# Optimization experiments

Measured on AMD Instinct MI355X. Metric: run time of the kernel, lower is better.

The kernel has to match this reference:

```python
import jax, jax.numpy as jnp
import numpy as np

B, N, K = 64, 128, 12
D_ATOM, D_NBR, D_NEW = 256, 320, 256
H, DK = 8, 32  # D_NEW = H * DK
LN_EPS = 1e-5
NEG_INF = -1e9


def setup_inputs() -> dict:
    key = jax.random.key(0)
    ks = jax.random.split(key, 10)
    atom_feature = jax.random.normal(ks[0], (B, N, D_ATOM), jnp.float32)
    atom_neighbor_feature = jax.random.normal(ks[1], (B, N, K, D_NBR), jnp.float32)
    # valid-neighbor masks from random neighbor counts in [1, K]
    counts = jax.random.randint(ks[2], (B, N), 1, K + 1)
    valid = (jnp.arange(K)[None, None, :] < counts[:, :, None]).astype(jnp.float32)
    atom_attend_mask = valid[..., None]                      # (B,N,K,1), 1=real neighbor
    atom_softmax_mask = (1.0 - valid[..., None]) * NEG_INF   # (B,N,K,1), additive
    # parameters
    s = 1.0 / np.sqrt(D_ATOM)
    W_atom = jax.random.uniform(ks[3], (D_ATOM, D_NEW), jnp.float32, -s, s)
    b_atom = jnp.zeros((D_NEW,), jnp.float32)
    s2 = 1.0 / np.sqrt(D_NBR)
    W_nbr = jax.random.uniform(ks[4], (D_NBR, D_NEW), jnp.float32, -s2, s2)
    b_nbr = jnp.zeros((D_NEW,), jnp.float32)
    s3 = 1.0 / np.sqrt(DK)
    w_align = jax.random.uniform(ks[5], (DK, 1), jnp.float32, -s3, s3)
    b_align = jnp.zeros((1,), jnp.float32)
    ln_gamma = jnp.ones((D_NEW,), jnp.float32)
    ln_beta = jnp.zeros((D_NEW,), jnp.float32)
    return dict(atom_feature=atom_feature, atom_neighbor_feature=atom_neighbor_feature,
                atom_softmax_mask=atom_softmax_mask, atom_attend_mask=atom_attend_mask,
                W_atom=W_atom, b_atom=b_atom, W_nbr=W_nbr, b_nbr=b_nbr,
                w_align=w_align, b_align=b_align, ln_gamma=ln_gamma, ln_beta=ln_beta)


def reference(atom_feature, atom_neighbor_feature, atom_softmax_mask, atom_attend_mask,
              W_atom, b_atom, W_nbr, b_nbr, w_align, b_align, ln_gamma, ln_beta):
    # dropout is identity at eval time
    h = atom_feature @ W_atom + b_atom                    # (B,N,D_NEW)
    e = atom_neighbor_feature @ W_nbr + b_nbr             # (B,N,K,D_NEW)
    h = h.reshape(B, N, 1, H, DK)                         # broadcast over K
    e = e.reshape(B, N, K, H, DK)
    # GATv2: act(h_i + e_j) then per-head linear score
    feat = jax.nn.leaky_relu(h + e)                       # slope 0.01 == torch default
    score = feat @ w_align + b_align                      # (B,N,K,H,1)
    score = score + atom_softmax_mask[:, :, :, None, :]   # additive -inf on pad
    attn = jax.nn.softmax(score, axis=2)                  # softmax over neighbors K
    attn = attn * atom_attend_mask[:, :, :, None, :]
    ctx = jnp.sum(attn * e, axis=2).reshape(B, N, H * DK)  # (B,N,D_NEW)
    # LayerNorm
    mu = jnp.mean(ctx, axis=-1, keepdims=True)
    xc = ctx - mu
    var = jnp.mean(xc * xc, axis=-1, keepdims=True)
    return xc * jax.lax.rsqrt(var + LN_EPS) * ln_gamma + ln_beta
```

## Files before the change

### kernel.cpp

```cpp
#include <hip/hip_runtime.h>

#define KN 12
#define DNBR 320
#define DNEW 256
#define BN_TOT 8192
#define ATB 4
#define HATB 16
#define NKS_E 10
#define NKS_H 8
#define ASTR_H 264
#define H_OFF 294912
#define NCHUNK 80

typedef short bf8_t __attribute__((ext_vector_type(8)));
typedef float f32x4 __attribute__((ext_vector_type(4)));
typedef unsigned short us8 __attribute__((ext_vector_type(8)));
using u16 = unsigned short;
using u32 = unsigned int;

typedef __attribute__((address_space(3))) void lds_vp;
typedef __attribute__((address_space(1))) const void gc_vp;

__device__ __forceinline__ void dma16(const void* g, void* l) {
    __builtin_amdgcn_global_load_lds((gc_vp*)g, (lds_vp*)l, 16, 0, 0);
}

__device__ __forceinline__ u16 f2bf(float f) {
    u32 x = __float_as_uint(f);
    return (u16)((x + 0x7fffu + ((x >> 16) & 1u)) >> 16);
}

__device__ __forceinline__ us8 pack8(float4 a, float4 b) {
    us8 v;
    v[0] = f2bf(a.x); v[1] = f2bf(a.y); v[2] = f2bf(a.z); v[3] = f2bf(a.w);
    v[4] = f2bf(b.x); v[5] = f2bf(b.y); v[6] = f2bf(b.z); v[7] = f2bf(b.w);
    return v;
}

__device__ __forceinline__ bf8_t cvt8(float4 a, float4 b) {
    u32 r0, r1, r2, r3;
    asm("v_cvt_pk_bf16_f32 %0, %1, %2" : "=v"(r0) : "v"(a.x), "v"(a.y));
    asm("v_cvt_pk_bf16_f32 %0, %1, %2" : "=v"(r1) : "v"(a.z), "v"(a.w));
    asm("v_cvt_pk_bf16_f32 %0, %1, %2" : "=v"(r2) : "v"(b.x), "v"(b.y));
    asm("v_cvt_pk_bf16_f32 %0, %1, %2" : "=v"(r3) : "v"(b.z), "v"(b.w));
    union { u32 u[4]; bf8_t v; } cv;
    cv.u[0] = r0; cv.u[1] = r1; cv.u[2] = r2; cv.u[3] = r3;
    return cv.v;
}

__global__ __launch_bounds__(256) void build_b2(
    const float* __restrict__ Wn, const float* __restrict__ Wa,
    u16* __restrict__ B2)
{
    int tile = blockIdx.x * 4 + (threadIdx.x >> 6);
    int l = threadIdx.x & 63;
    int q = l >> 4, m = l & 15;
    us8 v;
    if (tile < 160) {
        int ks = tile >> 4, nt = tile & 15;
        int col = nt * 16 + m;
#pragma unroll
        for (int e = 0; e < 8; e++)
            v[e] = f2bf(Wn[(ks * 32 + q * 8 + e) * DNEW + col]);
    } else {
        int tt = tile - 160;
        int ks = tt >> 4, nt = tt & 15;
        int col = nt * 16 + m;
#pragma unroll
        for (int e = 0; e < 8; e++)
            v[e] = f2bf(Wa[(ks * 32 + q * 8 + e) * DNEW + col]);
    }
    *(us8*)&B2[(size_t)tile * 512 + l * 8] = v;
}

__global__ __launch_bounds__(256) void h_pre(
    const float* __restrict__ atomf, const u16* __restrict__ B2,
    const float* __restrict__ ba, float* __restrict__ h_g)
{
    __shared__ u16 A[HATB * ASTR_H];

    const int t = threadIdx.x;
    const int l = t & 63, w = t >> 6, q = l >> 4, m = l & 15;
    const int ab = blockIdx.x * HATB;

    const float* base = atomf + (size_t)ab * DNEW;
    float4 u0 = *(const float4*)(base + t * 8);
    float4 u1 = *(const float4*)(base + t * 8 + 4);
    float4 u2 = *(const float4*)(base + (t + 256) * 8);
    float4 u3 = *(const float4*)(base + (t + 256) * 8 + 4);
    int ai = t >> 5, c8 = t & 31;
    *(us8*)&A[ai * ASTR_H + c8 * 8] = pack8(u0, u1);
    *(us8*)&A[(ai + 8) * ASTR_H + c8 * 8] = pack8(u2, u3);
    __syncthreads();

    f32x4 acc[4];
#pragma unroll
    for (int j = 0; j < 4; j++) acc[j] = (f32x4){0.f, 0.f, 0.f, 0.f};

#pragma unroll
    for (int ks = 0; ks < NKS_H; ks++) {
        bf8_t af = *(bf8_t*)&A[m * ASTR_H + ks * 32 + q * 8];
#pragma unroll
        for (int j = 0; j < 4; j++) {
            bf8_t bfj = *(const bf8_t*)&B2[((size_t)(160 + ks * 16 + w * 4 + j) * 64 + l) * 8];
            acc[j] = __builtin_amdgcn_mfma_f32_16x16x32_bf16(af, bfj, acc[j], 0, 0, 0);
        }
    }
#pragma unroll
    for (int j = 0; j < 4; j++) {
        int col = w * 64 + j * 16 + m;
        float bav = ba[col];
#pragma unroll
        for (int r = 0; r < 4; r++) {
            int row = ab + q * 4 + r;
            h_g[(size_t)row * DNEW + col] = acc[j][r] + bav;
        }
    }
}

__global__ __launch_bounds__(512, 4) void fused_all(
    const float* __restrict__ nbrf,
    const float* __restrict__ smaskg, const float* __restrict__ amaskg,
    const u16* __restrict__ B2, const float* __restrict__ h_g,
    const float* __restrict__ bnb, const float* __restrict__ walg,
    const float* __restrict__ balg, const float* __restrict__ gam,
    const float* __restrict__ bet, float* __restrict__ out)
{
    __shared__ __align__(16) float smem[NCHUNK * 256];

    const int t = threadIdx.x;
    const int l = t & 63, q = l >> 4, m = l & 15;
    const int w = __builtin_amdgcn_readfirstlane(t >> 6);
    const int a0 = blockIdx.x * ATB;
    const bool qv = (q < 3);
    const int srow = (m < KN) ? m : (KN - 1);

    for (int c = w; c < NCHUNK; c += 8) {
        int at = c / 20, rem = c - at * 20, ksc = rem >> 1, half = rem & 1;
        const float* src = nbrf + ((size_t)(a0 + at) * KN + srow) * DNBR
                         + ksc * 32 + q * 8 + half * 4;
        dma16(src, (char*)smem + (size_t)c * 1024);
    }

    const float bal = balg[0];
    float hv[ATB][2], bnbv[2], wv[2], gv[2], btv[2];
#pragma unroll
    for (int j = 0; j < 2; j++) {
        int col = w * 32 + j * 16 + m;
        bnbv[j] = bnb[col];
        wv[j] = walg[j * 16 + m];
        gv[j] = gam[col];
        btv[j] = bet[col];
#pragma unroll
        for (int at = 0; at < ATB; at++)
            hv[at][j] = h_g[(size_t)(a0 + at) * DNEW + col];
    }
    float smv[ATB][4], amv[ATB][4];
#pragma unroll
    for (int at = 0; at < ATB; at++)
#pragma unroll
        for (int r = 0; r < 4; r++) {
            int k = q * 4 + r;
            smv[at][r] = qv ? smaskg[(size_t)(a0 + at) * KN + k] + bal : 0.f;
            amv[at][r] = qv ? amaskg[(size_t)(a0 + at) * KN + k] : 0.f;
        }

    __syncthreads();

    const float4* A2 = (const float4*)smem;
    f32x4 acc_e[ATB][2];
#pragma unroll
    for (int at = 0; at < ATB; at++)
#pragma unroll
        for (int j = 0; j < 2; j++) acc_e[at][j] = (f32x4){0.f, 0.f, 0.f, 0.f};

#pragma unroll
    for (int ks = 0; ks < NKS_E; ks++) {
        bf8_t bfj[2];
#pragma unroll
        for (int j = 0; j < 2; j++)
            bfj[j] = *(const bf8_t*)&B2[((size_t)(ks * 16 + w * 2 + j) * 64 + l) * 8];
#pragma unroll
        for (int at = 0; at < ATB; at++) {
            float4 lo = A2[(size_t)((at * NKS_E + ks) * 2 + 0) * 64 + l];
            float4 hi = A2[(size_t)((at * NKS_E + ks) * 2 + 1) * 64 + l];
            bf8_t af = cvt8(lo, hi);
            acc_e[at][0] = __builtin_amdgcn_mfma_f32_16x16x32_bf16(af, bfj[0], acc_e[at][0], 0, 0, 0);
            acc_e[at][1] = __builtin_amdgcn_mfma_f32_16x16x32_bf16(af, bfj[1], acc_e[at][1], 0, 0, 0);
        }
    }

#pragma unroll
    for (int j = 0; j < 2; j++)
#pragma unroll
        for (int at = 0; at < ATB; at++)
#pragma unroll
            for (int r = 0; r < 4; r++) acc_e[at][j][r] += bnbv[j];

    float ctxv[ATB][2], s1s[ATB], s2s[ATB];
#pragma unroll
    for (int at = 0; at < ATB; at++) {
        float p[4];
#pragma unroll
        for (int r = 0; r < 4; r++) {
            float pp = 0.f;
#pragma unroll
            for (int j = 0; j < 2; j++) {
                float f = acc_e[at][j][r] + hv[at][j];
                f = f > 0.f ? f : 0.01f * f;
                pp = fmaf(f, wv[j], pp);
            }
            pp += __shfl_xor(pp, 1);
            pp += __shfl_xor(pp, 2);
            pp += __shfl_xor(pp, 4);
            pp += __shfl_xor(pp, 8);
            p[r] = qv ? pp + smv[at][r] : -1e30f;
        }
        float mx = fmaxf(fmaxf(p[0], p[1]), fmaxf(p[2], p[3]));
        mx = fmaxf(mx, __shfl_xor(mx, 16));
        mx = fmaxf(mx, __shfl_xor(mx, 32));
        float ex[4], ss = 0.f;
#pragma unroll
        for (int r = 0; r < 4; r++) {
            ex[r] = qv ? __expf(p[r] - mx) : 0.f;
            ss += ex[r];
        }
        ss += __shfl_xor(ss, 16);
        ss += __shfl_xor(ss, 32);
        float inv = 1.f / ss;
        float am[4];
#pragma unroll
        for (int r = 0; r < 4; r++)
            am[r] = qv ? ex[r] * inv * amv[at][r] : 0.f;
        float s1 = 0.f, s2 = 0.f;
#pragma unroll
        for (int j = 0; j < 2; j++) {
            float cp = am[0] * acc_e[at][j][0] + am[1] * acc_e[at][j][1] +
                       am[2] * acc_e[at][j][2] + am[3] * acc_e[at][j][3];
            cp += __shfl_xor(cp, 16);
            cp += __shfl_xor(cp, 32);
            ctxv[at][j] = cp;
            s1 += cp;
            s2 += cp * cp;
        }
#pragma unroll
        for (int off = 1; off < 16; off <<= 1) {
            s1 += __shfl_xor(s1, off);
            s2 += __shfl_xor(s2, off);
        }
        s1s[at] = s1; s2s[at] = s2;
    }

    float* red_l = smem;
    __syncthreads();
    if (l == 0) {
#pragma unroll
        for (int at = 0; at < ATB; at++) {
            red_l[at * 16 + w] = s1s[at];
            red_l[at * 16 + 8 + w] = s2s[at];
        }
    }
    __syncthreads();

#pragma unroll
    for (int at = 0; at < ATB; at++) {
        float ts1 = 0.f, ts2 = 0.f;
#pragma unroll
        for (int k = 0; k < 8; k++) {
            ts1 += red_l[at * 16 + k];
            ts2 += red_l[at * 16 + 8 + k];
        }
        float mu = ts1 * (1.f / 256.f);
        float var = ts2 * (1.f / 256.f) - mu * mu;
        var = fmaxf(var, 0.f);
        float rs = rsqrtf(var + 1e-5f);
        if (q == 0) {
#pragma unroll
            for (int j = 0; j < 2; j++) {
                int col = w * 32 + j * 16 + m;
                out[(size_t)(a0 + at) * DNEW + col] =
                    (ctxv[at][j] - mu) * rs * gv[j] + btv[j];
            }
        }
    }
}

extern "C" void kernel_launch(void* const* d_in, const int* in_sizes, int n_in,
                              void* d_out, int out_size, void* d_ws, size_t ws_size,
                              hipStream_t stream) {
    const float* atomf = (const float*)d_in[0];
    const float* nbrf  = (const float*)d_in[1];
    const float* smask = (const float*)d_in[2];
    const float* amask = (const float*)d_in[3];
    const float* Wa    = (const float*)d_in[4];
    const float* ba    = (const float*)d_in[5];
    const float* Wn    = (const float*)d_in[6];
    const float* bnb   = (const float*)d_in[7];
    const float* wal   = (const float*)d_in[8];
    const float* bal   = (const float*)d_in[9];
    const float* gam   = (const float*)d_in[10];
    const float* bet   = (const float*)d_in[11];
    float* outp = (float*)d_out;

    u16* B2 = (u16*)d_ws;
    float* h_g = (float*)((char*)d_ws + H_OFF);

    build_b2<<<72, 256, 0, stream>>>(Wn, Wa, B2);
    h_pre<<<BN_TOT / HATB, 256, 0, stream>>>(atomf, B2, ba, h_g);
    fused_all<<<BN_TOT / ATB, 512, 0, stream>>>(nbrf, smask, amask, B2, h_g,
                                                bnb, wal, bal, gam, bet, outp);
}
```

Measured before the change: 247.9 us.

## Assign one atom per wave in fused kernel, removing cross-wave LayerNorm reduction

The fused kernel now uses 256-thread blocks where each wave owns a whole atom and computes all 16 column tiles of the neighbor projection itself, rather than 8 waves splitting columns across 4 atoms. This removes the LDS-based cross-wave LayerNorm reduction and both block-level barriers, replacing __syncthreads with a per-wave vmcnt wait. In exchange each wave holds 16 accumulators and loads all 16 B fragments per k-step, raising register pressure and lowering occupancy (launch bounds now 256,2). The A-operand LDS layout and DMA mapping are also reorganised per wave.

```diff
diff --git a/kernel.cpp b/kernel.cpp
--- a/kernel.cpp
+++ b/kernel.cpp
@@ -10,7 +10,6 @@
 #define NKS_H 8
 #define ASTR_H 264
 #define H_OFF 294912
-#define NCHUNK 80
 
 typedef short bf8_t __attribute__((ext_vector_type(8)));
 typedef float f32x4 __attribute__((ext_vector_type(4)));
@@ -118,7 +117,7 @@
     }
 }
 
-__global__ __launch_bounds__(512, 4) void fused_all(
+__global__ __launch_bounds__(256, 2) void fused_all(
     const float* __restrict__ nbrf,
     const float* __restrict__ smaskg, const float* __restrict__ amaskg,
     const u16* __restrict__ B2, const float* __restrict__ h_g,
@@ -126,95 +125,92 @@
     const float* __restrict__ balg, const float* __restrict__ gam,
     const float* __restrict__ bet, float* __restrict__ out)
 {
-    __shared__ __align__(16) float smem[NCHUNK * 256];
+    __shared__ __align__(16) float smem[ATB * 20 * 256];
 
     const int t = threadIdx.x;
     const int l = t & 63, q = l >> 4, m = l & 15;
-    const int w = __builtin_amdgcn_readfirstlane(t >> 6);
-    const int a0 = blockIdx.x * ATB;
+    const int w = t >> 6;
+    const int atom = blockIdx.x * ATB + w;
     const bool qv = (q < 3);
+
+    const int cc = l >> 4;
     const int srow = (m < KN) ? m : (KN - 1);
-
-    for (int c = w; c < NCHUNK; c += 8) {
-        int at = c / 20, rem = c - at * 20, ksc = rem >> 1, half = rem & 1;
-        const float* src = nbrf + ((size_t)(a0 + at) * KN + srow) * DNBR
-                         + ksc * 32 + q * 8 + half * 4;
-        dma16(src, (char*)smem + (size_t)c * 1024);
+    const float* abase = nbrf + ((size_t)atom * KN + srow) * DNBR;
+    char* lbase = (char*)smem + (size_t)w * 20480;
+#pragma unroll
+    for (int c = 0; c < 20; c++) {
+        int ks = c >> 1, h = c & 1;
+        dma16(abase + ks * 32 + h * 16 + cc * 4, lbase + c * 1024);
     }
 
     const float bal = balg[0];
-    float hv[ATB][2], bnbv[2], wv[2], gv[2], btv[2];
-#pragma unroll
-    for (int j = 0; j < 2; j++) {
-        int col = w * 32 + j * 16 + m;
+    float hv[16], bnbv[16];
+#pragma unroll
+    for (int j = 0; j < 16; j++) {
+        int col = j * 16 + m;
+        hv[j] = h_g[(size_t)atom * DNEW + col];
         bnbv[j] = bnb[col];
-        wv[j] = walg[j * 16 + m];
-        gv[j] = gam[col];
-        btv[j] = bet[col];
-#pragma unroll
-        for (int at = 0; at < ATB; at++)
-            hv[at][j] = h_g[(size_t)(a0 + at) * DNEW + col];
-    }
-    float smv[ATB][4], amv[ATB][4];
-#pragma unroll
-    for (int at = 0; at < ATB; at++)
-#pragma unroll
-        for (int r = 0; r < 4; r++) {
-            int k = q * 4 + r;
-            smv[at][r] = qv ? smaskg[(size_t)(a0 + at) * KN + k] + bal : 0.f;
-            amv[at][r] = qv ? amaskg[(size_t)(a0 + at) * KN + k] : 0.f;
-        }
-
-    __syncthreads();
-
-    const float4* A2 = (const float4*)smem;
-    f32x4 acc_e[ATB][2];
-#pragma unroll
-    for (int at = 0; at < ATB; at++)
-#pragma unroll
-        for (int j = 0; j < 2; j++) acc_e[at][j] = (f32x4){0.f, 0.f, 0.f, 0.f};
+    }
+    float wv2[2] = { walg[m], walg[16 + m] };
+    float smv[4], amv[4];
+#pragma unroll
+    for (int r = 0; r < 4; r++) {
+        int k = q * 4 + r;
+        smv[r] = qv ? smaskg[(size_t)atom * KN + k] + bal : 0.f;
+        amv[r] = qv ? amaskg[(size_t)atom * KN + k] : 0.f;
+    }
+
+    asm volatile("s_waitcnt vmcnt(0)" ::: "memory");
+    __builtin_amdgcn_sched_barrier(0);
+
+    const float4* A2w = (const float4*)lbase;
+    const bf8_t* B2v = (const bf8_t*)B2;
+    const int aoff = (q & 1) * 32 + m;
+    const int hsel = q >> 1;
+
+    f32x4 acc[16];
+#pragma unroll
+    for (int j = 0; j < 16; j++) acc[j] = (f32x4){0.f, 0.f, 0.f, 0.f};
 
 #pragma unroll
     for (int ks = 0; ks < NKS_E; ks++) {
-        bf8_t bfj[2];
-#pragma unroll
-        for (int j = 0; j < 2; j++)
-            bfj[j] = *(const bf8_t*)&B2[((size_t)(ks * 16 + w * 2 + j) * 64 + l) * 8];
-#pragma unroll
-        for (int at = 0; at < ATB; at++) {
-            float4 lo = A2[(size_t)((at * NKS_E + ks) * 2 + 0) * 64 + l];
-            float4 hi = A2[(size_t)((at * NKS_E + ks) * 2 + 1) * 64 + l];
-            bf8_t af = cvt8(lo, hi);
-            acc_e[at][0] = __builtin_amdgcn_mfma_f32_16x16x32_bf16(af, bfj[0], acc_e[at][0], 0, 0, 0);
-            acc_e[at][1] = __builtin_amdgcn_mfma_f32_16x16x32_bf16(af, bfj[1], acc_e[at][1], 0, 0, 0);
-        }
-    }
-
-#pragma unroll
-    for (int j = 0; j < 2; j++)
-#pragma unroll
-        for (int at = 0; at < ATB; at++)
-#pragma unroll
-            for (int r = 0; r < 4; r++) acc_e[at][j][r] += bnbv[j];
-
-    float ctxv[ATB][2], s1s[ATB], s2s[ATB];
-#pragma unroll
-    for (int at = 0; at < ATB; at++) {
+        bf8_t bfj[16];
+#pragma unroll
+        for (int j = 0; j < 16; j++)
+            bfj[j] = B2v[(size_t)(ks * 16 + j) * 64 + l];
+        float4 lo = A2w[(ks * 2 + hsel) * 64 + aoff];
+        float4 hi = A2w[(ks * 2 + hsel) * 64 + aoff + 16];
+        bf8_t af = cvt8(lo, hi);
+#pragma unroll
+        for (int j = 0; j < 16; j++)
+            acc[j] = __builtin_amdgcn_mfma_f32_16x16x32_bf16(af, bfj[j], acc[j], 0, 0, 0);
+    }
+
+#pragma unroll
+    for (int j = 0; j < 16; j++)
+#pragma unroll
+        for (int r = 0; r < 4; r++) acc[j][r] += bnbv[j];
+
+    float ctxv[16];
+    float s1 = 0.f, s2 = 0.f;
+#pragma unroll
+    for (int u = 0; u < 8; u++) {
+        const int j0 = 2 * u, j1 = 2 * u + 1;
         float p[4];
 #pragma unroll
         for (int r = 0; r < 4; r++) {
             float pp = 0.f;
-#pragma unroll
-            for (int j = 0; j < 2; j++) {
-                float f = acc_e[at][j][r] + hv[at][j];
-                f = f > 0.f ? f : 0.01f * f;
-                pp = fmaf(f, wv[j], pp);
-            }
+            float f0 = acc[j0][r] + hv[j0];
+            f0 = f0 > 0.f ? f0 : 0.01f * f0;
+            pp = fmaf(f0, wv2[0], pp);
+            float f1 = acc[j1][r] + hv[j1];
+            f1 = f1 > 0.f ? f1 : 0.01f * f1;
+            pp = fmaf(f1, wv2[1], pp);
             pp += __shfl_xor(pp, 1);
             pp += __shfl_xor(pp, 2);
             pp += __shfl_xor(pp, 4);
             pp += __shfl_xor(pp, 8);
-            p[r] = qv ? pp + smv[at][r] : -1e30f;
+            p[r] = qv ? pp + smv[r] : -1e30f;
         }
         float mx = fmaxf(fmaxf(p[0], p[1]), fmaxf(p[2], p[3]));
         mx = fmaxf(mx, __shfl_xor(mx, 16));
@@ -231,57 +227,35 @@
         float am[4];
 #pragma unroll
         for (int r = 0; r < 4; r++)
-            am[r] = qv ? ex[r] * inv * amv[at][r] : 0.f;
-        float s1 = 0.f, s2 = 0.f;
-#pragma unroll
-        for (int j = 0; j < 2; j++) {
-            float cp = am[0] * acc_e[at][j][0] + am[1] * acc_e[at][j][1] +
-                       am[2] * acc_e[at][j][2] + am[3] * acc_e[at][j][3];
+            am[r] = qv ? ex[r] * inv * amv[r] : 0.f;
+#pragma unroll
+        for (int jo = 0; jo < 2; jo++) {
+            int j = 2 * u + jo;
+            float cp = am[0] * acc[j][0] + am[1] * acc[j][1] +
+                       am[2] * acc[j][2] + am[3] * acc[j][3];
             cp += __shfl_xor(cp, 16);
             cp += __shfl_xor(cp, 32);
-            ctxv[at][j] = cp;
+            ctxv[j] = cp;
             s1 += cp;
             s2 += cp * cp;
         }
-#pragma unroll
-        for (int off = 1; off < 16; off <<= 1) {
-            s1 += __shfl_xor(s1, off);
-            s2 += __shfl_xor(s2, off);
-        }
-        s1s[at] = s1; s2s[at] = s2;
-    }
-
-    float* red_l = smem;
-    __syncthreads();
-    if (l == 0) {
-#pragma unroll
-        for (int at = 0; at < ATB; at++) {
-            red_l[at * 16 + w] = s1s[at];
-            red_l[at * 16 + 8 + w] = s2s[at];
-        }
-    }
-    __syncthreads();
-
-#pragma unroll
-    for (int at = 0; at < ATB; at++) {
-        float ts1 = 0.f, ts2 = 0.f;
-#pragma unroll
-        for (int k = 0; k < 8; k++) {
-            ts1 += red_l[at * 16 + k];
-            ts2 += red_l[at * 16 + 8 + k];
-        }
-        float mu = ts1 * (1.f / 256.f);
-        float var = ts2 * (1.f / 256.f) - mu * mu;
-        var = fmaxf(var, 0.f);
-        float rs = rsqrtf(var + 1e-5f);
-        if (q == 0) {
-#pragma unroll
-            for (int j = 0; j < 2; j++) {
-                int col = w * 32 + j * 16 + m;
-                out[(size_t)(a0 + at) * DNEW + col] =
-                    (ctxv[at][j] - mu) * rs * gv[j] + btv[j];
-            }
-        }
+    }
+#pragma unroll
+    for (int off = 1; off < 16; off <<= 1) {
+        s1 += __shfl_xor(s1, off);
+        s2 += __shfl_xor(s2, off);
+    }
+    float mu = s1 * (1.f / 256.f);
+    float var = s2 * (1.f / 256.f) - mu * mu;
+    var = fmaxf(var, 0.f);
+    float rs = rsqrtf(var + 1e-5f);
+
+#pragma unroll
+    for (int jj = 0; jj < 4; jj++) {
+        int j = q * 4 + jj;
+        int col = j * 16 + m;
+        out[(size_t)atom * DNEW + col] =
+            (ctxv[j] - mu) * rs * gam[col] + bet[col];
     }
 }
 
@@ -307,6 +281,6 @@
 
     build_b2<<<72, 256, 0, stream>>>(Wn, Wa, B2);
     h_pre<<<BN_TOT / HATB, 256, 0, stream>>>(atomf, B2, ba, h_g);
-    fused_all<<<BN_TOT / ATB, 512, 0, stream>>>(nbrf, smask, amask, B2, h_g,
+    fused_all<<<BN_TOT / ATB, 256, 0, stream>>>(nbrf, smask, amask, B2, h_g,
                                                 bnb, wal, bal, gam, bet, outp);
 }
```

Result: slower. 263.8 us (+6.4%).
